# Kernel optimization log

Measured on AMD Instinct MI355X. Metric: run time of the kernel, lower is better.

## Reference

```python
import jax, jax.numpy as jnp
import numpy as np

T, B, C, U = 4000, 64, 64, 200
NEG_INF = jnp.float32(-1e30)


def setup_inputs() -> dict:
    key = jax.random.key(0)
    k1, k2 = jax.random.split(key)
    inputs = jax.random.normal(k1, (T, B, C), dtype=jnp.float32)  # time-major logits
    targets = jax.random.randint(k2, (B, U), 0, C, dtype=jnp.int32)
    return {"inputs": inputs, "targets": targets}


def reference(inputs, targets):
    # Transducer.forward: transitions is None -> log_softmax over classes.
    log_probs = jax.nn.log_softmax(inputs, axis=-1)  # [T, B, C]
    # emit[t, b, u] = log_probs[t, b, targets[b, u]]
    b_idx = jnp.arange(B)[:, None]  # [B, 1]
    emit = log_probs[:, b_idx, targets]  # [T, B, U]

    # ASG-style monotone alignment forward DP (no blank, repeats collapse):
    # alpha[t, u] = emit[t, u] + logsumexp(alpha[t-1, u], alpha[t-1, u-1])
    alpha0 = jnp.full((B, U), NEG_INF, dtype=inputs.dtype).at[:, 0].set(emit[0, :, 0])

    def step(alpha, emit_t):
        shifted = jnp.concatenate(
            [jnp.full((B, 1), NEG_INF, dtype=alpha.dtype), alpha[:, :-1]], axis=1
        )
        return emit_t + jnp.logaddexp(alpha, shifted), None

    alpha_T, _ = jax.lax.scan(step, alpha0, emit[1:])  # scan over T-1 frames
    losses = -alpha_T[:, U - 1]  # negated forward score per sample
    return jnp.mean(losses)  # TransducerLossFunction returns torch.mean(loss)
```

## Files before the change

kernel.cpp:

```cpp
#include <hip/hip_runtime.h>

#define T_DIM 4000
#define B_DIM 64
#define C_DIM 64
#define U_DIM 200
#define LOG2E 1.4426950408889634f
#define LN2 0.6931471805599453f

#define PAIRS 2000
#define PB_BYTES (PAIRS * 800)
#define NSLOT 20
#define HALF 10

__device__ __forceinline__ float hw_exp2(float x) { return __builtin_amdgcn_exp2f(x); }
__device__ __forceinline__ float hw_log2(float x) { return __builtin_amdgcn_logf(x); }

template <int CTRL>
__device__ __forceinline__ int dpp_i(int x) {
    return __builtin_amdgcn_update_dpp(0, x, CTRL, 0xF, 0xF, true);
}
template <int CTRL>
__device__ __forceinline__ float dpp_f(float x) {
    return __uint_as_float((unsigned)dpp_i<CTRL>((int)__float_as_uint(x)));
}

__device__ __forceinline__ unsigned rne_bf16(float v) {
    unsigned b = __float_as_uint(v);
    return b + 0x7FFFu + ((b >> 16) & 1u);
}

__global__ __launch_bounds__(256, 8) void prep_kernel(const float* __restrict__ in,
                                                      const int* __restrict__ tgt,
                                                      unsigned* __restrict__ eg,
                                                      float* __restrict__ out) {
    __shared__ unsigned short exh[16 * 8 * 68];
    __shared__ unsigned tgc[400];
    __shared__ float red[4];
    const int tid = threadIdx.x;
    const int bg = blockIdx.x & 7;
    const int tc = blockIdx.x >> 3;
    const int t0 = tc * 16, b0 = bg * 8;

    for (int o = tid; o < 400; o += 256) {
        int4 tv = ((const int4*)tgt)[bg * 400 + o];
        tgc[o] = (unsigned)(tv.x & 63) | ((unsigned)(tv.y & 63) << 8)
               | ((unsigned)(tv.z & 63) << 16) | ((unsigned)(tv.w & 63) << 24);
    }
    #pragma unroll
    for (int k = 0; k < 8; ++k) {
        int flat = k * 256 + tid;
        int t_l = flat >> 7, i = flat & 127, b_l = i >> 4, q = i & 15;
        float4 v = *(const float4*)(in + (size_t)(t0 + t_l) * 4096 + (b0 + b_l) * 64 + q * 4);
        unsigned ex0 = rne_bf16(hw_exp2(v.x * LOG2E));
        unsigned ex1 = rne_bf16(hw_exp2(v.y * LOG2E));
        unsigned ex2 = rne_bf16(hw_exp2(v.z * LOG2E));
        unsigned ex3 = rne_bf16(hw_exp2(v.w * LOG2E));
        uint2 pk;
        pk.x = (ex0 >> 16) | (ex1 & 0xFFFF0000u);
        pk.y = (ex2 >> 16) | (ex3 & 0xFFFF0000u);
        *(uint2*)&exh[(t_l * 8 + b_l) * 68 + q * 4] = pk;
    }
    __syncthreads();

    {
        float v = 0.0f;
        if (tid < 128) {
            const unsigned* p = (const unsigned*)&exh[tid * 68];
            float s = 0.0f;
            #pragma unroll
            for (int j = 0; j < 32; ++j) {
                unsigned u = p[j];
                s += __uint_as_float(u << 16) + __uint_as_float(u & 0xFFFF0000u);
            }
            v = hw_log2(s);
        }
        #pragma unroll
        for (int o = 32; o > 0; o >>= 1) v += __shfl_xor(v, o);
        if ((tid & 63) == 0) red[tid >> 6] = v;
    }

    {
        const int wv4 = tid >> 6;
        const int ln = tid & 63;
        for (int r = wv4; r < 64; r += 4) {
            int b_l = r & 7, tp_l = r >> 3;
            if (ln < 50) {
                unsigned tw = tgc[b_l * 50 + ln];
                int c0 = tw & 255, c1 = (tw >> 8) & 255, c2 = (tw >> 16) & 255, c3 = tw >> 24;
                const unsigned short* plo = &exh[(tp_l * 16 + b_l) * 68];
                const unsigned short* phi = plo + 8 * 68;
                uint4 w;
                w.x = (unsigned)plo[c0] | ((unsigned)plo[c1] << 16);
                w.y = (unsigned)plo[c2] | ((unsigned)plo[c3] << 16);
                w.z = (unsigned)phi[c0] | ((unsigned)phi[c1] << 16);
                w.w = (unsigned)phi[c2] | ((unsigned)phi[c3] << 16);
                *(uint4*)((char*)eg + (size_t)(b0 + b_l) * PB_BYTES
                          + (size_t)(tc * 8 + tp_l) * 800 + ln * 16) = w;
            }
        }
    }
    __syncthreads();
    if (tid == 0)
        atomicAdd(out, (red[0] + red[1] + red[2] + red[3]) * (LN2 / 64.0f));
}

struct ScanState { float A0, A1, A2, A3; int S, D; };

__device__ __forceinline__ void renorm(ScanState& st, int lane) {
    float m = fmaxf(fmaxf(st.A0, st.A1), fmaxf(st.A2, st.A3));
    int e = (int)((__float_as_uint(m) >> 23) & 0xFFu);
    int cand = st.S + e - 127;
    int snb = dpp_i<0x138>(st.S);
    if (lane == 0) snb = -(1 << 28);
    int snew = max(cand, snb);
    int k = st.S - snew;
    st.A0 = ldexpf(st.A0, k);
    st.A1 = ldexpf(st.A1, k);
    st.A2 = ldexpf(st.A2, k);
    st.A3 = ldexpf(st.A3, k);
    st.S = snew;
    st.D = min(dpp_i<0x138>(snew) - snew, 60);
}

__device__ __forceinline__ void step(ScanState& st, float e0, float e1, float e2, float e3) {
    float sh = ldexpf(dpp_f<0x138>(st.A3), st.D);
    sh = fminf(sh, 1.125899906842624e15f);
    float t0 = st.A0 + sh;
    float t1 = st.A1 + st.A0;
    float t2 = st.A2 + st.A1;
    float t3 = st.A3 + st.A2;
    st.A0 = e0 * t0; st.A1 = e1 * t1; st.A2 = e2 * t2; st.A3 = e3 * t3;
}

__device__ __forceinline__ void brenorm(ScanState& st) {
    float m = fmaxf(fmaxf(st.A0, st.A1), fmaxf(st.A2, st.A3));
    int e = (int)((__float_as_uint(m) >> 23) & 0xFFu);
    int cand = st.S + e - 127;
    int snb = dpp_i<0x130>(st.S);
    int snew = max(cand, snb);
    int k = st.S - snew;
    st.A0 = ldexpf(st.A0, k);
    st.A1 = ldexpf(st.A1, k);
    st.A2 = ldexpf(st.A2, k);
    st.A3 = ldexpf(st.A3, k);
    st.S = snew;
    st.D = min(dpp_i<0x130>(snew) - snew, 60);
}

__device__ __forceinline__ void bstep(ScanState& st, float e0, float e1, float e2, float e3) {
    float e4s = fminf(ldexpf(dpp_f<0x130>(e0), st.D), 1.125899906842624e15f);
    float b0n = dpp_f<0x130>(st.A0);
    float g0 = e0 * st.A0, g1 = e1 * st.A1, g2 = e2 * st.A2, g3 = e3 * st.A3;
    st.A0 = g0 + g1; st.A1 = g1 + g2; st.A2 = g2 + g3; st.A3 = g3 + e4s * b0n;
}

__device__ __forceinline__ ScanState scan_init(const float* in, const int* tgt, int lane, int b) {
    float v0 = in[b * 64 + (tgt[b * U_DIM] & 63)];
    ScanState st;
    st.A0 = (lane == 0) ? hw_exp2(v0 * LOG2E) : 0.0f;
    st.A1 = 0.0f; st.A2 = 0.0f; st.A3 = 0.0f;
    st.S = 0; st.D = 0;
    return st;
}

#define LO(x) __uint_as_float((x) << 16)
#define HI(x) __uint_as_float((x) & 0xFFFF0000u)

__global__ __launch_bounds__(128, 1) void scan2_kernel(const float* __restrict__ in,
                                                       const int* __restrict__ tgt,
                                                       const unsigned* __restrict__ eg,
                                                       float* __restrict__ out) {
    __shared__ float jb0[64], jb1[64], jb2[64], jb3[64];
    __shared__ int jsb[64];
    const int lane = threadIdx.x & 63;
    const int wv = threadIdx.x >> 6;
    const int b = blockIdx.x;
    const int lidx = (lane < 50) ? lane : 49;
    const char* egb = (const char*)eg + (size_t)b * PB_BYTES;

    ScanState st;
    if (wv == 1) {
        st.A0 = 0.0f; st.A1 = 0.0f; st.A2 = 0.0f;
        st.A3 = (lane == 49) ? 1.0f : 0.0f;
        st.S = 0; st.D = 0;
        int off = 1999 * 800 + lidx * 16;
        uint4 wb[NSLOT];
        #pragma unroll
        for (int j = 0; j < NSLOT; ++j) { wb[j] = *(const uint4*)(egb + off); off -= 800; }
        for (int k = 0; k < 49; ++k) {
            #pragma unroll
            for (int j = 0; j < HALF; ++j) {
                if ((j & 3) == 0) brenorm(st);
                uint4 w = wb[j];
                bstep(st, LO(w.z), HI(w.z), LO(w.w), HI(w.w));
                bstep(st, LO(w.x), HI(w.x), LO(w.y), HI(w.y));
            }
            #pragma unroll
            for (int j = 0; j < HALF; ++j) { wb[j] = *(const uint4*)(egb + off); off -= 800; }
            #pragma unroll
            for (int j = HALF; j < NSLOT; ++j) {
                if ((j & 3) == 0) brenorm(st);
                uint4 w = wb[j];
                bstep(st, LO(w.z), HI(w.z), LO(w.w), HI(w.w));
                bstep(st, LO(w.x), HI(w.x), LO(w.y), HI(w.y));
            }
            #pragma unroll
            for (int j = HALF; j < NSLOT; ++j) { wb[j] = *(const uint4*)(egb + off); off -= 800; }
        }
        #pragma unroll
        for (int j = 0; j < NSLOT; ++j) {
            if ((j & 3) == 0) brenorm(st);
            uint4 w = wb[j];
            bstep(st, LO(w.z), HI(w.z), LO(w.w), HI(w.w));
            if (j < NSLOT - 1) bstep(st, LO(w.x), HI(w.x), LO(w.y), HI(w.y));
        }
        brenorm(st);
        jb0[lane] = st.A0; jb1[lane] = st.A1; jb2[lane] = st.A2; jb3[lane] = st.A3;
        jsb[lane] = st.S;
    } else {
        st = scan_init(in, tgt, lane, b);
        int off = 800 + lidx * 16;
        uint4 wb[NSLOT];
        #pragma unroll
        for (int j = 0; j < NSLOT; ++j) { wb[j] = *(const uint4*)(egb + off); off += 800; }
        uint2 h0 = *(const uint2*)(egb + lidx * 16 + 8);
        step(st, LO(h0.x), HI(h0.x), LO(h0.y), HI(h0.y));
        for (int k = 0; k < 49; ++k) {
            #pragma unroll
            for (int j = 0; j < HALF; ++j) {
                if ((j & 3) == 0) renorm(st, lane);
                uint4 w = wb[j];
                step(st, LO(w.x), HI(w.x), LO(w.y), HI(w.y));
                step(st, LO(w.z), HI(w.z), LO(w.w), HI(w.w));
            }
            #pragma unroll
            for (int j = 0; j < HALF; ++j) { wb[j] = *(const uint4*)(egb + off); off += 800; }
            #pragma unroll
            for (int j = HALF; j < NSLOT; ++j) {
                if ((j & 3) == 0) renorm(st, lane);
                uint4 w = wb[j];
                step(st, LO(w.x), HI(w.x), LO(w.y), HI(w.y));
                step(st, LO(w.z), HI(w.z), LO(w.w), HI(w.w));
            }
            #pragma unroll
            for (int j = HALF; j < NSLOT; ++j) { wb[j] = *(const uint4*)(egb + off); off += 800; }
        }
        #pragma unroll
        for (int j = 0; j < NSLOT; ++j) {
            if ((j & 3) == 0) renorm(st, lane);
            uint4 w = wb[j];
            step(st, LO(w.x), HI(w.x), LO(w.y), HI(w.y));
            if (j < NSLOT - 1) step(st, LO(w.z), HI(w.z), LO(w.w), HI(w.w));
        }
        renorm(st, lane);
    }
    __syncthreads();
    if (wv == 0) {
        float d = st.A0 * jb0[lane] + st.A1 * jb1[lane]
                + st.A2 * jb2[lane] + st.A3 * jb3[lane];
        float ll = (lane < 50) ? hw_log2(fmaxf(d, 1e-38f)) + (float)(st.S + jsb[lane])
                               : -1e30f;
        float mx = ll;
        #pragma unroll
        for (int o = 32; o > 0; o >>= 1) mx = fmaxf(mx, __shfl_xor(mx, o));
        float s = (lane < 50) ? hw_exp2(ll - mx) : 0.0f;
        #pragma unroll
        for (int o = 32; o > 0; o >>= 1) s += __shfl_xor(s, o);
        if (lane == 0) atomicAdd(out, -(mx + hw_log2(s)) * (LN2 / 64.0f));
    }
}

__global__ __launch_bounds__(256) void lse_sum_kernel(const float* __restrict__ in,
                                                      float* __restrict__ out) {
    const int lane = threadIdx.x & 63;
    const int w = threadIdx.x >> 6;
    const int wid = blockIdx.x * 4 + w;
    const int ROWS = (T_DIM * B_DIM) / 1024;
    const float* p = in + (size_t)wid * ROWS * 64 + lane;
    float acc = 0.0f;
    for (int i = 0; i < ROWS; i += 2) {
        float xa = p[(size_t)i * 64];
        float xb = p[(size_t)(i + 1) * 64];
        float ea = hw_exp2(xa * LOG2E);
        float eb = hw_exp2(xb * LOG2E);
        #pragma unroll
        for (int off = 32; off > 0; off >>= 1) {
            ea += __shfl_xor(ea, off);
            eb += __shfl_xor(eb, off);
        }
        acc += hw_log2(ea) + hw_log2(eb);
    }
    __shared__ float red[4];
    if (lane == 0) red[w] = acc;
    __syncthreads();
    if (threadIdx.x == 0)
        atomicAdd(out, (red[0] + red[1] + red[2] + red[3]) * (LN2 / 64.0f));
}

__global__ __launch_bounds__(64) void scan_fb(const float* __restrict__ in,
                                              const int* __restrict__ tgt,
                                              float* __restrict__ out) {
    const int lane = threadIdx.x;
    const int b = blockIdx.x;
    const int lidx = (lane < 50) ? lane : 49;
    int4 tg = ((const int4*)(tgt + b * U_DIM))[lidx];
    tg.x &= 63; tg.y &= 63; tg.z &= 63; tg.w &= 63;
    ScanState st = scan_init(in, tgt, lane, b);
    const char* inb = (const char*)in;
    int o0 = 16384 + b * 256 + tg.x * 4;
    int o1 = 16384 + b * 256 + tg.y * 4;
    int o2 = 16384 + b * 256 + tg.z * 4;
    int o3 = 16384 + b * 256 + tg.w * 4;
    const int m0 = 3999 * 16384 + b * 256 + tg.x * 4;
    const int m1 = m0 + (tg.y - tg.x) * 4;
    const int m2 = m0 + (tg.z - tg.x) * 4;
    const int m3 = m0 + (tg.w - tg.x) * 4;
    float f0[16], f1[16], f2[16], f3[16];
    #pragma unroll
    for (int j = 0; j < 16; ++j) {
        f0[j] = *(const float*)(inb + min(o0, m0)); o0 += 16384;
        f1[j] = *(const float*)(inb + min(o1, m1)); o1 += 16384;
        f2[j] = *(const float*)(inb + min(o2, m2)); o2 += 16384;
        f3[j] = *(const float*)(inb + min(o3, m3)); o3 += 16384;
    }
    for (int k = 0; k < 249; ++k) {
        #pragma unroll
        for (int j = 0; j < 16; ++j) {
            if (j == 0 || j == 8) renorm(st, lane);
            float e0 = hw_exp2(f0[j] * LOG2E);
            float e1 = hw_exp2(f1[j] * LOG2E);
            float e2 = hw_exp2(f2[j] * LOG2E);
            float e3 = hw_exp2(f3[j] * LOG2E);
            f0[j] = *(const float*)(inb + min(o0, m0)); o0 += 16384;
            f1[j] = *(const float*)(inb + min(o1, m1)); o1 += 16384;
            f2[j] = *(const float*)(inb + min(o2, m2)); o2 += 16384;
            f3[j] = *(const float*)(inb + min(o3, m3)); o3 += 16384;
            step(st, e0, e1, e2, e3);
        }
    }
    #pragma unroll
    for (int j = 0; j < 15; ++j) {
        if (j == 0 || j == 8) renorm(st, lane);
        float e0 = hw_exp2(f0[j] * LOG2E);
        float e1 = hw_exp2(f1[j] * LOG2E);
        float e2 = hw_exp2(f2[j] * LOG2E);
        float e3 = hw_exp2(f3[j] * LOG2E);
        step(st, e0, e1, e2, e3);
    }
    if (lane == 49) {
        float a2 = hw_log2(fmaxf(st.A3, 1e-38f)) + (float)st.S;
        atomicAdd(out, -a2 * (LN2 / 64.0f));
    }
}

extern "C" void kernel_launch(void* const* d_in, const int* in_sizes, int n_in,
                              void* d_out, int out_size, void* d_ws, size_t ws_size,
                              hipStream_t stream) {
    const float* inputs = (const float*)d_in[0];
    const int* targets = (const int*)d_in[1];
    float* out = (float*)d_out;

    (void)hipMemsetAsync(out, 0, sizeof(float), stream);

    const size_t eg_bytes = (size_t)B_DIM * PB_BYTES;
    if (ws_size >= eg_bytes) {
        unsigned* eg = (unsigned*)d_ws;
        prep_kernel<<<2000, 256, 0, stream>>>(inputs, targets, eg, out);
        scan2_kernel<<<B_DIM, 128, 0, stream>>>(inputs, targets, eg, out);
    } else {
        scan_fb<<<B_DIM, 64, 0, stream>>>(inputs, targets, out);
        lse_sum_kernel<<<256, 256, 0, stream>>>(inputs, out);
    }
}
```

Baseline: 187.0 us.

## Fuse two forward DP steps using precomputed pairwise emission products

The prep kernel now stores, for forward-half time pairs, the products of consecutive-frame emissions (bf16), so the forward scan can advance two frames per combined update (fstep2) with a shorter dependency chain and fewer cross-lane shuffles per pair. The backward half keeps the original per-step form. The high bf16 half is also used without masking the low bits, which drops an AND per element but lets the packed neighbour bits perturb the value slightly. The extra rounding of the products in bf16 and the second clamped shift may change accuracy.

```diff
diff --git a/kernel.cpp b/kernel.cpp
--- a/kernel.cpp
+++ b/kernel.cpp
@@ -11,6 +11,7 @@
 #define PB_BYTES (PAIRS * 800)
 #define NSLOT 20
 #define HALF 10
+#define CLAMP50 1.125899906842624e15f
 
 __device__ __forceinline__ float hw_exp2(float x) { return __builtin_amdgcn_exp2f(x); }
 __device__ __forceinline__ float hw_log2(float x) { return __builtin_amdgcn_logf(x); }
@@ -27,6 +28,10 @@
 __device__ __forceinline__ unsigned rne_bf16(float v) {
     unsigned b = __float_as_uint(v);
     return b + 0x7FFFu + ((b >> 16) & 1u);
+}
+
+__device__ __forceinline__ float ldh(unsigned short u) {
+    return __uint_as_float((unsigned)u << 16);
 }
 
 __global__ __launch_bounds__(256, 8) void prep_kernel(const float* __restrict__ in,
@@ -84,18 +89,32 @@
         const int ln = tid & 63;
         for (int r = wv4; r < 64; r += 4) {
             int b_l = r & 7, tp_l = r >> 3;
+            int tp = tc * 8 + tp_l;
             if (ln < 50) {
                 unsigned tw = tgc[b_l * 50 + ln];
                 int c0 = tw & 255, c1 = (tw >> 8) & 255, c2 = (tw >> 16) & 255, c3 = tw >> 24;
                 const unsigned short* plo = &exh[(tp_l * 16 + b_l) * 68];
                 const unsigned short* phi = plo + 8 * 68;
                 uint4 w;
-                w.x = (unsigned)plo[c0] | ((unsigned)plo[c1] << 16);
-                w.y = (unsigned)plo[c2] | ((unsigned)plo[c3] << 16);
-                w.z = (unsigned)phi[c0] | ((unsigned)phi[c1] << 16);
-                w.w = (unsigned)phi[c2] | ((unsigned)phi[c3] << 16);
+                if (tp == 0 || tp >= 1000) {
+                    w.x = (unsigned)plo[c0] | ((unsigned)plo[c1] << 16);
+                    w.y = (unsigned)plo[c2] | ((unsigned)plo[c3] << 16);
+                    w.z = (unsigned)phi[c0] | ((unsigned)phi[c1] << 16);
+                    w.w = (unsigned)phi[c2] | ((unsigned)phi[c3] << 16);
+                } else {
+                    int cm1 = ln ? (int)(tgc[b_l * 50 + ln - 1] >> 24) : c0;
+                    float a0 = ldh(plo[c0]), a1 = ldh(plo[c1]);
+                    float a2 = ldh(plo[c2]), a3 = ldh(plo[c3]);
+                    float am = ldh(plo[cm1]);
+                    float b0v = ldh(phi[c0]), b1v = ldh(phi[c1]);
+                    float b2v = ldh(phi[c2]), b3v = ldh(phi[c3]);
+                    w.x = (rne_bf16(b0v * a0) >> 16) | (rne_bf16(b1v * a1) & 0xFFFF0000u);
+                    w.y = (rne_bf16(b2v * a2) >> 16) | (rne_bf16(b3v * a3) & 0xFFFF0000u);
+                    w.z = (rne_bf16(b0v * am) >> 16) | (rne_bf16(b1v * a0) & 0xFFFF0000u);
+                    w.w = (rne_bf16(b2v * a1) >> 16) | (rne_bf16(b3v * a2) & 0xFFFF0000u);
+                }
                 *(uint4*)((char*)eg + (size_t)(b0 + b_l) * PB_BYTES
-                          + (size_t)(tc * 8 + tp_l) * 800 + ln * 16) = w;
+                          + (size_t)tp * 800 + ln * 16) = w;
             }
         }
     }
@@ -124,7 +143,7 @@
 
 __device__ __forceinline__ void step(ScanState& st, float e0, float e1, float e2, float e3) {
     float sh = ldexpf(dpp_f<0x138>(st.A3), st.D);
-    sh = fminf(sh, 1.125899906842624e15f);
+    sh = fminf(sh, CLAMP50);
     float t0 = st.A0 + sh;
     float t1 = st.A1 + st.A0;
     float t2 = st.A2 + st.A1;
@@ -148,10 +167,28 @@
 }
 
 __device__ __forceinline__ void bstep(ScanState& st, float e0, float e1, float e2, float e3) {
-    float e4s = fminf(ldexpf(dpp_f<0x130>(e0), st.D), 1.125899906842624e15f);
+    float e4s = fminf(ldexpf(dpp_f<0x130>(e0), st.D), CLAMP50);
     float b0n = dpp_f<0x130>(st.A0);
     float g0 = e0 * st.A0, g1 = e1 * st.A1, g2 = e2 * st.A2, g3 = e3 * st.A3;
     st.A0 = g0 + g1; st.A1 = g1 + g2; st.A2 = g2 + g3; st.A3 = g3 + e4s * b0n;
+}
+
+__device__ __forceinline__ void fstep2(ScanState& st, const uint4& w) {
+    float F0 = __uint_as_float(w.x << 16), F1 = __uint_as_float(w.x);
+    float F2 = __uint_as_float(w.y << 16), F3 = __uint_as_float(w.y);
+    float G0 = __uint_as_float(w.z << 16), G1 = __uint_as_float(w.z);
+    float G2 = __uint_as_float(w.w << 16), G3 = __uint_as_float(w.w);
+    float sh3 = fminf(ldexpf(dpp_f<0x138>(st.A3), st.D), CLAMP50);
+    float sh2 = fminf(ldexpf(dpp_f<0x138>(st.A2), st.D), CLAMP50);
+    float sm1 = sh3 + sh2;
+    float s0 = st.A0 + sh3;
+    float s1 = st.A1 + st.A0;
+    float s2 = st.A2 + st.A1;
+    float s3 = st.A3 + st.A2;
+    st.A0 = F0 * s0 + G0 * sm1;
+    st.A1 = F1 * s1 + G1 * s0;
+    st.A2 = F2 * s2 + G2 * s1;
+    st.A3 = F3 * s3 + G3 * s2;
 }
 
 __device__ __forceinline__ ScanState scan_init(const float* in, const int* tgt, int lane, int b) {
@@ -164,7 +201,8 @@
 }
 
 #define LO(x) __uint_as_float((x) << 16)
-#define HI(x) __uint_as_float((x) & 0xFFFF0000u)
+#define HIx(x) __uint_as_float(x)
+#define HIm(x) __uint_as_float((x) & 0xFFFF0000u)
 
 __global__ __launch_bounds__(128, 1) void scan2_kernel(const float* __restrict__ in,
                                                        const int* __restrict__ tgt,
@@ -192,8 +230,8 @@
             for (int j = 0; j < HALF; ++j) {
                 if ((j & 3) == 0) brenorm(st);
                 uint4 w = wb[j];
-                bstep(st, LO(w.z), HI(w.z), LO(w.w), HI(w.w));
-                bstep(st, LO(w.x), HI(w.x), LO(w.y), HI(w.y));
+                bstep(st, LO(w.z), HIx(w.z), LO(w.w), HIx(w.w));
+                bstep(st, LO(w.x), HIx(w.x), LO(w.y), HIx(w.y));
             }
             #pragma unroll
             for (int j = 0; j < HALF; ++j) { wb[j] = *(const uint4*)(egb + off); off -= 800; }
@@ -201,8 +239,8 @@
             for (int j = HALF; j < NSLOT; ++j) {
                 if ((j & 3) == 0) brenorm(st);
                 uint4 w = wb[j];
-                bstep(st, LO(w.z), HI(w.z), LO(w.w), HI(w.w));
-                bstep(st, LO(w.x), HI(w.x), LO(w.y), HI(w.y));
+                bstep(st, LO(w.z), HIx(w.z), LO(w.w), HIx(w.w));
+                bstep(st, LO(w.x), HIx(w.x), LO(w.y), HIx(w.y));
             }
             #pragma unroll
             for (int j = HALF; j < NSLOT; ++j) { wb[j] = *(const uint4*)(egb + off); off -= 800; }
@@ -211,8 +249,8 @@
         for (int j = 0; j < NSLOT; ++j) {
             if ((j & 3) == 0) brenorm(st);
             uint4 w = wb[j];
-            bstep(st, LO(w.z), HI(w.z), LO(w.w), HI(w.w));
-            if (j < NSLOT - 1) bstep(st, LO(w.x), HI(w.x), LO(w.y), HI(w.y));
+            bstep(st, LO(w.z), HIx(w.z), LO(w.w), HIx(w.w));
+            if (j < NSLOT - 1) bstep(st, LO(w.x), HIx(w.x), LO(w.y), HIx(w.y));
         }
         brenorm(st);
         jb0[lane] = st.A0; jb1[lane] = st.A1; jb2[lane] = st.A2; jb3[lane] = st.A3;
@@ -224,14 +262,13 @@
         #pragma unroll
         for (int j = 0; j < NSLOT; ++j) { wb[j] = *(const uint4*)(egb + off); off += 800; }
         uint2 h0 = *(const uint2*)(egb + lidx * 16 + 8);
-        step(st, LO(h0.x), HI(h0.x), LO(h0.y), HI(h0.y));
+        step(st, LO(h0.x), HIx(h0.x), LO(h0.y), HIx(h0.y));
         for (int k = 0; k < 49; ++k) {
             #pragma unroll
             for (int j = 0; j < HALF; ++j) {
                 if ((j & 3) == 0) renorm(st, lane);
                 uint4 w = wb[j];
-                step(st, LO(w.x), HI(w.x), LO(w.y), HI(w.y));
-                step(st, LO(w.z), HI(w.z), LO(w.w), HI(w.w));
+                fstep2(st, w);
             }
             #pragma unroll
             for (int j = 0; j < HALF; ++j) { wb[j] = *(const uint4*)(egb + off); off += 800; }
@@ -239,8 +276,7 @@
             for (int j = HALF; j < NSLOT; ++j) {
                 if ((j & 3) == 0) renorm(st, lane);
                 uint4 w = wb[j];
-                step(st, LO(w.x), HI(w.x), LO(w.y), HI(w.y));
-                step(st, LO(w.z), HI(w.z), LO(w.w), HI(w.w));
+                fstep2(st, w);
             }
             #pragma unroll
             for (int j = HALF; j < NSLOT; ++j) { wb[j] = *(const uint4*)(egb + off); off += 800; }
@@ -249,8 +285,8 @@
         for (int j = 0; j < NSLOT; ++j) {
             if ((j & 3) == 0) renorm(st, lane);
             uint4 w = wb[j];
-            step(st, LO(w.x), HI(w.x), LO(w.y), HI(w.y));
-            if (j < NSLOT - 1) step(st, LO(w.z), HI(w.z), LO(w.w), HI(w.w));
+            if (j < NSLOT - 1) fstep2(st, w);
+            else step(st, LO(w.x), HIx(w.x), LO(w.y), HIx(w.y));
         }
         renorm(st, lane);
     }
```

Result: slower. 191.7 us (+2.5%).
